# Kernel tuning notes

Hardware: AMD Instinct MI355X
Metric: run time of the kernel (lower is better)

Reference implementation:

```python
import jax, jax.numpy as jnp
import numpy as np
from jax.scipy.special import gammainc

ALPH = 0.8  # significance level (default arg in original forward)


def _median_width(X, iu, ju):
    # pairwise squared distances; original takes median of strictly-positive
    # strict-upper-triangle entries (tril subtracted) -> median over triu(k=1)
    G = jnp.sum(X * X, axis=1)                    # [n]
    D = G[:, None] + G[None, :] - 2.0 * (X @ X.T)  # [n, n]
    du = D[iu, ju]                                 # strict upper triangle, static size
    return jnp.sqrt(0.5 * jnp.median(du))


def _rbf(X, width):
    G = jnp.sum(X * X, axis=1)
    D = G[:, None] + G[None, :] - 2.0 * (X @ X.T)
    return jnp.exp(-D / (2.0 * width ** 2))


def _center(K):
    # H K H with H = I - 11^T/n  ==  K - rowmean - colmean + totalmean
    cm = jnp.mean(K, axis=0, keepdims=True)   # mean over rows  -> [1, n]
    rm = jnp.mean(K, axis=1, keepdims=True)   # mean over cols  -> [n, 1]
    tm = jnp.mean(K)
    return K - cm - rm + tm


def _gamma_ppf(a, p):
    # invert regularized lower incomplete gamma via fixed-iteration bisection
    hi0 = a + 10.0 * jnp.sqrt(a) + 100.0
    def body(i, lohi):
        lo, hi = lohi
        mid = 0.5 * (lo + hi)
        below = gammainc(a, mid) < p
        return (jnp.where(below, mid, lo), jnp.where(below, hi, mid))
    lo, hi = jax.lax.fori_loop(0, 100, body, (jnp.zeros_like(a), hi0))
    return 0.5 * (lo + hi)


def setup_inputs() -> dict:
    key = jax.random.key(0)
    k1, k2 = jax.random.split(key)
    X = jax.random.normal(k1, (4096, 64), dtype=jnp.float32)
    Y = jax.random.normal(k2, (4096, 64), dtype=jnp.float32)
    return {"X": X, "Y": Y}


def reference(X, Y):
    n = X.shape[0]
    iu, ju = np.triu_indices(n, k=1)  # static index set

    width_x = _median_width(X, iu, ju)
    width_y = _median_width(Y, iu, ju)

    K = _rbf(X, width_x)
    L = _rbf(Y, width_y)

    Kc = _center(K)
    Lc = _center(L)

    testStat = jnp.sum(Kc.T * Lc) / n

    V = (Kc * Lc / 6.0) ** 2
    varHSIC = (jnp.sum(V) - jnp.trace(V)) / n / (n - 1)
    varHSIC = varHSIC * 72.0 * (n - 4) * (n - 5) / n / (n - 1) / (n - 2) / (n - 3)

    # zero-diagonal kernels for mean estimate
    K0sum = jnp.sum(K) - jnp.trace(K)
    L0sum = jnp.sum(L) - jnp.trace(L)
    muX = K0sum / n / (n - 1)
    muY = L0sum / n / (n - 1)
    mHSIC = (1.0 + muX * muY - muX - muY) / n

    al = mHSIC ** 2 / varHSIC
    bet = varHSIC * n / mHSIC
    thresh = bet * _gamma_ppf(al, jnp.float32(1.0 - ALPH))
    return (testStat, thresh)
```

## Files before the change

### kernel.cpp

```cpp
#include <hip/hip_runtime.h>

typedef unsigned int u32;
typedef unsigned short u16;
typedef __attribute__((ext_vector_type(8))) short bf16x8;
typedef __attribute__((ext_vector_type(4))) float f32x4;

#define NPTS 4096
#define DIM  64
#define NB   32
#define NBLK 528
#define WLO16 0x4140u
#define NWBIN 832
#define RSTR 836


__device__ __forceinline__ void bmap(int b, int& by, int& bx){
  by = 0;
  while (b >= NB - by){ b -= NB - by; by++; }
  bx = by + b;
}

__device__ __forceinline__ u16 f2bf(float x){
  u32 u = __float_as_uint(x);
  return (u16)((u + 0x7fffu + ((u>>16)&1u)) >> 16);
}

__global__ __launch_bounds__(256) void convert_k(const float* __restrict__ X, const float* __restrict__ Y,
                                                 u16* __restrict__ Xbf, float* __restrict__ Gall,
                                                 u32* __restrict__ histsum, double* __restrict__ rowK,
                                                 double* __restrict__ rowL, double* __restrict__ sums){
  int t = blockIdx.x*256 + threadIdx.x;
  int rid = t >> 1, hf = t & 1;
  int z = rid >> 12, row = rid & 4095;
  const float* src = (z ? Y : X) + (size_t)row*DIM + hf*32;
  u16* base = Xbf + ((size_t)z*32768 + (size_t)(row>>4)*128 + (row&15))*8;
  float g = 0.f;
#pragma unroll
  for (int f=0; f<4; f++){
    float4 f0 = *(const float4*)(src + f*8);
    float4 f1 = *(const float4*)(src + f*8 + 4);
    g = fmaf(f0.x,f0.x,g); g = fmaf(f0.y,f0.y,g); g = fmaf(f0.z,f0.z,g); g = fmaf(f0.w,f0.w,g);
    g = fmaf(f1.x,f1.x,g); g = fmaf(f1.y,f1.y,g); g = fmaf(f1.z,f1.z,g); g = fmaf(f1.w,f1.w,g);
    ushort4 h0, h1;
    h0.x=f2bf(f0.x); h0.y=f2bf(f0.y); h0.z=f2bf(f0.z); h0.w=f2bf(f0.w);
    h1.x=f2bf(f1.x); h1.y=f2bf(f1.y); h1.z=f2bf(f1.z); h1.w=f2bf(f1.w);
    u16* dst = base + (size_t)(hf*4 + f)*16*8;
    *(ushort4*)dst = h0;
    *(ushort4*)(dst+4) = h1;
  }
  g += __shfl_xor(g, 1, 64);
  if (hf==0) Gall[rid] = g;
  if (t < NPTS){ rowK[t] = 0.0; rowL[t] = 0.0; }
  if (t < 2*RSTR) histsum[t] = 0u;
  if (t < 2) sums[t] = 0.0;
}

__global__ __launch_bounds__(256,2) void hist_k(const u16* __restrict__ Xbf, const float* __restrict__ Gall,
                                                u32* __restrict__ histsum){
  __shared__ u32 lh[RSTR];
  int z = blockIdx.y, tid = threadIdx.x;
  int by,bx; bmap(blockIdx.x, by, bx);
  bool isdiag = (by==bx);
  u32 wgt = isdiag ? 1u : 2u;
  int w=tid>>6, lane=tid&63, q=lane>>4, nl=lane&15;
  for (int t=tid;t<RSTR;t+=256) lh[t]=0;
  __syncthreads();
  const bf16x8* Xb = (const bf16x8*)Xbf + (size_t)z*32768;
  const float* Gz = Gall + z*NPTS;
  int rt0 = w, rt1 = 4 + w;
  int ag0 = by*8 + rt0, ag1 = by*8 + rt1;
  bf16x8 a0f0 = Xb[ag0*128 + q*16 + nl];
  bf16x8 a0f1 = Xb[ag0*128 + (4+q)*16 + nl];
  bf16x8 a1f0 = Xb[ag1*128 + q*16 + nl];
  bf16x8 a1f1 = Xb[ag1*128 + (4+q)*16 + nl];
  float ga0 = Gz[ag0*16 + nl], ga1 = Gz[ag1*16 + nl];
  float g0m[4], g1m[4];
#pragma unroll
  for (int r=0;r<4;r++){ g0m[r] = __shfl(ga0, q*4+r, 64); g1m[r] = __shfl(ga1, q*4+r, 64); }
#pragma unroll
  for (int tb=0;tb<8;tb++){
    int jg = bx*8 + tb;
    bf16x8 bf0 = Xb[jg*128 + q*16 + nl];
    bf16x8 bf1 = Xb[jg*128 + (4+q)*16 + nl];
    f32x4 acc0 = (f32x4)0.0f, acc1 = (f32x4)0.0f;
    acc0 = __builtin_amdgcn_mfma_f32_16x16x32_bf16(a0f0, bf0, acc0, 0,0,0);
    acc0 = __builtin_amdgcn_mfma_f32_16x16x32_bf16(a0f1, bf1, acc0, 0,0,0);
    acc1 = __builtin_amdgcn_mfma_f32_16x16x32_bf16(a1f0, bf0, acc1, 0,0,0);
    acc1 = __builtin_amdgcn_mfma_f32_16x16x32_bf16(a1f1, bf1, acc1, 0,0,0);
    int j = jg*16 + nl;
    float gb = Gz[j];
#pragma unroll
    for (int r=0;r<4;r++){
      float d0 = (g0m[r] + gb) - 2.0f*acc0[r];
      float d1 = (g1m[r] + gb) - 2.0f*acc1[r];
      if (isdiag){
        if (ag0*16 + q*4 + r == j) d0 = 0.f;
        if (ag1*16 + q*4 + r == j) d1 = 0.f;
      }
      u32 t0 = __float_as_uint(d0) >> 16;
      u32 b0 = (t0 < WLO16) ? 0u : (t0 >= WLO16+NWBIN) ? (u32)(NWBIN+1) : (t0 - WLO16 + 1u);
      atomicAdd(&lh[b0], wgt);
      u32 t1 = __float_as_uint(d1) >> 16;
      u32 b1 = (t1 < WLO16) ? 0u : (t1 >= WLO16+NWBIN) ? (u32)(NWBIN+1) : (t1 - WLO16 + 1u);
      atomicAdd(&lh[b1], wgt);
    }
  }
  __syncthreads();
  u32* dst = histsum + (size_t)z*RSTR;
  for (int t=tid;t<RSTR;t+=256){
    u32 v = lh[t];
    if (v) atomicAdd(&dst[t], v);
  }
}

__global__ __launch_bounds__(256) void scan16i(const u32* __restrict__ histsum,
                                               float* __restrict__ scal,
                                               u32 kf1, u32 kf2){
  int z = blockIdx.x;
  int tid = threadIdx.x;
  __shared__ u32 wsum[4];
  __shared__ double svals[2];
  u32 c4[4] = {0,0,0,0};
  if (tid < 209){
    const u32* base = histsum + (size_t)z*RSTR + 4*tid;
    int lim = RSTR - 4*tid;
    c4[0] = base[0];
    if (lim>1) c4[1] = base[1];
    if (lim>2) c4[2] = base[2];
    if (lim>3) c4[3] = base[3];
  }
  u32 s = c4[0]+c4[1]+c4[2]+c4[3];
  int lane = tid & 63, wv = tid >> 6;
  u32 pre = s;
#pragma unroll
  for (int off=1; off<64; off<<=1){
    u32 t2 = __shfl_up(pre, off, 64);
    if (lane >= off) pre += t2;
  }
  if (lane==63) wsum[wv] = pre;
  __syncthreads();
  u32 base2 = 0;
  for (int k=0;k<wv;k++) base2 += wsum[k];
  u32 incl = base2 + pre, excl = incl - s;
  u32 ks[2] = {kf1,kf2};
#pragma unroll
  for (int w2=0; w2<2; w2++){
    if (ks[w2] >= excl && ks[w2] < incl){
      u32 acc = excl;
#pragma unroll
      for (int j=0;j<4;j++){
        if (ks[w2] < acc + c4[j]){
          int b = tid*4 + j;
          double lo, hi;
          if (b==0){ lo=12.0; hi=12.0; }
          else if (b>=NWBIN+1){ lo=1024.0; hi=1024.0; }
          else {
            u32 t16 = WLO16 + (u32)b - 1u;
            lo = (double)__uint_as_float(t16<<16);
            hi = (double)__uint_as_float((t16+1u)<<16);
          }
          double frac = ((double)(ks[w2]-acc) + 0.5)/(double)c4[j];
          svals[w2] = lo + (hi-lo)*frac;
          break;
        }
        acc += c4[j];
      }
    }
  }
  __syncthreads();
  if (tid==0){
    float med = (float)(0.5*(svals[0]+svals[1]));
    float wd = sqrtf(0.5f*med);
    scal[z] = 2.0f*wd*wd;
  }
}

__global__ __launch_bounds__(256,2) void rowsum_k(const u16* __restrict__ Xbf, const float* __restrict__ Gall,
                                                  const float* __restrict__ scal,
                                                  double* __restrict__ rowK, double* __restrict__ rowL,
                                                  double* __restrict__ sums){
  __shared__ double rowacc[128];
  __shared__ double colLDS[4][128];
  __shared__ double tred[2];
  int z = blockIdx.y, tid = threadIdx.x;
  int by,bx; bmap(blockIdx.x, by, bx);
  bool isdiag = (by==bx);
  int w=tid>>6, lane=tid&63, q=lane>>4, nl=lane&15;
  const bf16x8* Xb = (const bf16x8*)Xbf + (size_t)z*32768;
  const float* Gz = Gall + z*NPTS;
  float negi = -1.0f/scal[z];
  int rt0 = w, rt1 = 4 + w;
  int ag0 = by*8 + rt0, ag1 = by*8 + rt1;
  bf16x8 a0f0 = Xb[ag0*128 + q*16 + nl];
  bf16x8 a0f1 = Xb[ag0*128 + (4+q)*16 + nl];
  bf16x8 a1f0 = Xb[ag1*128 + q*16 + nl];
  bf16x8 a1f1 = Xb[ag1*128 + (4+q)*16 + nl];
  float ga0 = Gz[ag0*16 + nl], ga1 = Gz[ag1*16 + nl];
  float g0m[4], g1m[4];
#pragma unroll
  for (int r=0;r<4;r++){ g0m[r] = __shfl(ga0, q*4+r, 64); g1m[r] = __shfl(ga1, q*4+r, 64); }
  double rs0[4] = {0,0,0,0}, rs1[4] = {0,0,0,0};
#pragma unroll
  for (int tb=0;tb<8;tb++){
    int jg = bx*8 + tb;
    bf16x8 bf0 = Xb[jg*128 + q*16 + nl];
    bf16x8 bf1 = Xb[jg*128 + (4+q)*16 + nl];
    f32x4 acc0 = (f32x4)0.0f, acc1 = (f32x4)0.0f;
    acc0 = __builtin_amdgcn_mfma_f32_16x16x32_bf16(a0f0, bf0, acc0, 0,0,0);
    acc0 = __builtin_amdgcn_mfma_f32_16x16x32_bf16(a0f1, bf1, acc0, 0,0,0);
    acc1 = __builtin_amdgcn_mfma_f32_16x16x32_bf16(a1f0, bf0, acc1, 0,0,0);
    acc1 = __builtin_amdgcn_mfma_f32_16x16x32_bf16(a1f1, bf1, acc1, 0,0,0);
    int j = jg*16 + nl;
    float gb = Gz[j];
    double cs = 0.0;
#pragma unroll
    for (int r=0;r<4;r++){
      float d0 = (g0m[r] + gb) - 2.0f*acc0[r];
      float d1 = (g1m[r] + gb) - 2.0f*acc1[r];
      if (isdiag){
        if (ag0*16 + q*4 + r == j) d0 = 0.f;
        if (ag1*16 + q*4 + r == j) d1 = 0.f;
      }
      double e0 = (double)expf(d0*negi);
      double e1 = (double)expf(d1*negi);
      rs0[r] += e0; rs1[r] += e1;
      cs += e0 + e1;
    }
    cs += __shfl_xor(cs, 16, 64);
    cs += __shfl_xor(cs, 32, 64);
    if (q==0) colLDS[w][tb*16 + nl] = cs;
  }
#pragma unroll
  for (int r=0;r<4;r++){
    double v0 = rs0[r], v1 = rs1[r];
    v0 += __shfl_xor(v0,1,64); v0 += __shfl_xor(v0,2,64);
    v0 += __shfl_xor(v0,4,64); v0 += __shfl_xor(v0,8,64);
    v1 += __shfl_xor(v1,1,64); v1 += __shfl_xor(v1,2,64);
    v1 += __shfl_xor(v1,4,64); v1 += __shfl_xor(v1,8,64);
    rs0[r] = v0; rs1[r] = v1;
  }
  if (nl==0){
#pragma unroll
    for (int r=0;r<4;r++){
      rowacc[rt0*16 + q*4 + r] = rs0[r];
      rowacc[rt1*16 + q*4 + r] = rs1[r];
    }
  }
  __syncthreads();
  double tot = 0.0;
  if (tid < 128){
    double rv = rowacc[tid];
    double cv = colLDS[0][tid] + colLDS[1][tid] + colLDS[2][tid] + colLDS[3][tid];
    double* rowG = z ? rowL : rowK;
    atomicAdd(&rowG[by*128 + tid], rv);
    if (!isdiag) atomicAdd(&rowG[bx*128 + tid], cv);
    tot = rv + (isdiag ? 0.0 : cv);
  }
#pragma unroll
  for (int s2=1;s2<64;s2<<=1) tot += __shfl_xor(tot, s2, 64);
  if (lane==0 && w<2) tred[w] = tot;
  __syncthreads();
  if (tid==0) atomicAdd(&sums[z], tred[0] + tred[1]);
}

__global__ __launch_bounds__(256,2) void final_k(const u16* __restrict__ Xbf, const float* __restrict__ Gall,
                                                 const float* __restrict__ scal,
                                                 const double* __restrict__ rowK,
                                                 const double* __restrict__ rowL,
                                                 const double* __restrict__ sums,
                                                 double* __restrict__ partials){
  int tid = threadIdx.x;
  int b = blockIdx.x >> 1, half = blockIdx.x & 1;
  int by,bx; bmap(b,by,bx);
  bool isdiag = (by==bx);
  int w=tid>>6, lane=tid&63, q=lane>>4, nl=lane&15;
  const bf16x8* Xb = (const bf16x8*)Xbf;
  const bf16x8* Yb = Xb + 32768;
  const float* Gx = Gall;
  const float* Gy = Gall + NPTS;
  const double inv_n = 1.0/(double)NPTS;
  double tmK = sums[0]*(inv_n*inv_n), tmL = sums[1]*(inv_n*inv_n);
  float negx = -1.0f/scal[0], negy = -1.0f/scal[1];
  double wgt = isdiag ? 1.0 : 2.0;
  double S1=0, S2=0, trV=0;
  int rt = half*4 + w;
  int ag = by*8 + rt;
  bf16x8 axf0 = Xb[ag*128 + q*16 + nl];
  bf16x8 axf1 = Xb[ag*128 + (4+q)*16 + nl];
  bf16x8 ayf0 = Yb[ag*128 + q*16 + nl];
  bf16x8 ayf1 = Yb[ag*128 + (4+q)*16 + nl];
  int rowA = ag*16 + nl;
  float gaX = Gx[rowA], gaY = Gy[rowA];
  float gXm[4], gYm[4];
#pragma unroll
  for (int r=0;r<4;r++){ gXm[r] = __shfl(gaX, q*4+r, 64); gYm[r] = __shfl(gaY, q*4+r, 64); }
  double rmKi[4], rmLi[4];
#pragma unroll
  for (int r=0;r<4;r++){
    int i = ag*16 + q*4 + r;
    rmKi[r] = rowK[i]*inv_n; rmLi[r] = rowL[i]*inv_n;
  }
#pragma unroll
  for (int tb=0;tb<8;tb++){
    int jg = bx*8 + tb;
    f32x4 accX = (f32x4)0.0f, accY = (f32x4)0.0f;
    accX = __builtin_amdgcn_mfma_f32_16x16x32_bf16(axf0, Xb[jg*128 + q*16 + nl],     accX, 0,0,0);
    accX = __builtin_amdgcn_mfma_f32_16x16x32_bf16(axf1, Xb[jg*128 + (4+q)*16 + nl], accX, 0,0,0);
    accY = __builtin_amdgcn_mfma_f32_16x16x32_bf16(ayf0, Yb[jg*128 + q*16 + nl],     accY, 0,0,0);
    accY = __builtin_amdgcn_mfma_f32_16x16x32_bf16(ayf1, Yb[jg*128 + (4+q)*16 + nl], accY, 0,0,0);
    int j = jg*16 + nl;
    float gbX = Gx[j], gbY = Gy[j];
    double cmK = rowK[j]*inv_n - tmK;
    double cmL = rowL[j]*inv_n - tmL;
#pragma unroll
    for (int r=0;r<4;r++){
      int i = ag*16 + q*4 + r;
      float dx = (gXm[r] + gbX) - 2.0f*accX[r];
      float dy = (gYm[r] + gbY) - 2.0f*accY[r];
      bool dg = isdiag && i==j;
      if (dg){ dx = 0.f; dy = 0.f; }
      float kx = expf(dx*negx);
      float lv = expf(dy*negy);
      double kc = ((double)kx - rmKi[r]) - cmK;
      double lc = ((double)lv - rmLi[r]) - cmL;
      double prod = kc*lc;
      S1 += wgt*prod;
      double vv = (prod*prod)*(1.0/36.0);
      S2 += wgt*vv;
      if (dg) trV += vv;
    }
  }
  __shared__ double red[4][3];
  double vals[3]={S1,S2,trV};
  int wv = tid >> 6;
#pragma unroll
  for (int v=0;v<3;v++){
    double x = vals[v];
#pragma unroll
    for (int s2=1;s2<64;s2<<=1) x += __shfl_xor(x, s2, 64);
    if (lane==0) red[wv][v]=x;
  }
  __syncthreads();
  if (tid < 3)
    partials[(size_t)blockIdx.x*4 + tid] = red[0][tid]+red[1][tid]+red[2][tid]+red[3][tid];
}

__device__ double gammainc_wave(double a, double x, double lga, int lane){
  double C = 1.0/a;
  double psum = 0.0;
  for (int b=0;b<8192;b++){
    double k = (double)(b*64 + lane + 1);
    double rr = x/(a+k);
    double pp = rr;
#pragma unroll
    for (int s=1;s<64;s<<=1){
      double t = __shfl_up(pp, s, 64);
      if (lane >= s) pp *= t;
    }
    double c = C*pp;
    psum += c;
    double clast = __shfl(c, 63, 64);
    double rlast = __shfl(rr, 63, 64);
    C = clast;
    if (rlast < 1.0 && clast*rlast/(1.0-rlast) < 1e-17) break;
  }
#pragma unroll
  for (int s=1;s<64;s<<=1) psum += __shfl_xor(psum, s, 64);
  double total = 1.0/a + psum;
  return exp(-x + a*log(x) - lga) * total;
}

__global__ __launch_bounds__(256) void finalize_k(const double* __restrict__ partials,
                                                  const double* __restrict__ sums,
                                                  float* __restrict__ out)
{
  __shared__ double red[3][4];
  __shared__ double tot[4];
  int tid = threadIdx.x;
  double v0=0,v1=0,v2=0;
  for (int i=tid; i<2*NBLK; i+=256){
    const double* p = partials + (size_t)i*4;
    v0+=p[0]; v1+=p[1]; v2+=p[2];
  }
  double vals[3]={v0,v1,v2};
  int lane = tid & 63, wv = tid >> 6;
#pragma unroll
  for (int v=0;v<3;v++){
    double x = vals[v];
#pragma unroll
    for (int s2=1;s2<64;s2<<=1) x += __shfl_xor(x, s2, 64);
    if (lane==0) red[v][wv]=x;
  }
  __syncthreads();
  if (tid==0){
#pragma unroll
    for (int v=0;v<3;v++) tot[v] = red[v][0]+red[v][1]+red[v][2]+red[v][3];
  }
  __syncthreads();
  if (tid >= 64) return;

  const double n = (double)NPTS;
  double totK=sums[0], totL=sums[1];
  double S1=tot[0], S2=tot[1], trV=tot[2];
  double testStat = S1/n;
  double varHSIC = (S2 - trV)/n/(n-1.0);
  varHSIC = varHSIC*72.0*(n-4.0)*(n-5.0)/n/(n-1.0)/(n-2.0)/(n-3.0);
  double muX = (totK-n)/n/(n-1.0);
  double muY = (totL-n)/n/(n-1.0);
  double mHSIC = (1.0 + muX*muY - muX - muY)/n;
  double al = mHSIC*mHSIC/varHSIC;
  double bet = varHSIC*n/mHSIC;
  double p = (double)((float)(1.0-0.8));
  double lga = lgamma(al);
  double lo = 0.0, hi = al + 10.0*sqrt(al) + 100.0;
  const double zp = -0.8416212335729142957;
  double t = 1.0 - 1.0/(9.0*al) + zp/(3.0*sqrt(al));
  double x = al*t*t*t;
  if (!(x > 0.0) || !(x < hi)) x = 0.5*hi;
  for (int it=0; it<2; ++it){
    double P = gammainc_wave(al, x, lga, lane);
    double diff = P - p;
    if (diff < 0.0) lo = x; else hi = x;
    if (fabs(diff) < 1e-12) break;
    double pdf = exp(-x + (al-1.0)*log(x) - lga);
    double nx = x - diff/pdf;
    if (!(nx > lo) || !(nx < hi)) nx = 0.5*(lo+hi);
    x = nx;
  }
  if (lane==0){
    out[0]=(float)testStat;
    out[1]=(float)(bet*x);
  }
}

extern "C" void kernel_launch(void* const* d_in, const int* in_sizes, int n_in,
                              void* d_out, int out_size, void* d_ws, size_t ws_size,
                              hipStream_t stream) {
  const float* X = (const float*)d_in[0];
  const float* Y = (const float*)d_in[1];
  float* out = (float*)d_out;
  char* ws = (char*)d_ws;

  double* sums     = (double*)ws;
  float*  scal     = (float*)(ws + 128);
  u32*    histsum  = (u32*)(ws + 256);
  double* rowK     = (double*)(ws + 8192);
  double* rowL     = (double*)(ws + 40960);
  float*  Gall     = (float*)(ws + 73728);
  double* partials = (double*)(ws + 106496);
  u16*    Xbf      = (u16*)(ws + (4u<<20));
  size_t need = (size_t)(4u<<20) + (size_t)2*NPTS*DIM*2;

  if (ws_size < need) return;

  const u32 KF1 = 4096u + 2u*4193279u;
  const u32 KF2 = 4096u + 2u*4193280u;

  convert_k<<<64,256,0,stream>>>(X, Y, Xbf, Gall, histsum, rowK, rowL, sums);
  hist_k<<<dim3(NBLK,2),256,0,stream>>>(Xbf, Gall, histsum);
  scan16i<<<2,256,0,stream>>>(histsum, scal, KF1, KF2);
  rowsum_k<<<dim3(NBLK,2),256,0,stream>>>(Xbf, Gall, scal, rowK, rowL, sums);
  final_k<<<2*NBLK,256,0,stream>>>(Xbf, Gall, scal, rowK, rowL, sums, partials);
  finalize_k<<<1,256,0,stream>>>(partials, sums, out);
}
```

Measured before the change: 146.9 us.

## Fuse six HSIC kernels into one cooperative persistent kernel with grid syncs

Replaces the chain of separate launches (convert, histogram, scan, rowsum, final, finalize) with a single cooperative kernel. Stages are separated by grid-wide barriers and work items are distributed over a persistent grid sized from occupancy. This removes per-launch overhead and inter-kernel gaps. In exchange, grid.sync costs are added, occupancy is fixed at a grid that may be smaller than the original work count, and all phases share one union of shared memory.

```diff
diff --git a/kernel.cpp b/kernel.cpp
--- a/kernel.cpp
+++ b/kernel.cpp
@@ -1,4 +1,7 @@
 #include <hip/hip_runtime.h>
+#include <hip/hip_cooperative_groups.h>
+
+namespace cg = cooperative_groups;
 
 typedef unsigned int u32;
 typedef unsigned short u16;
@@ -12,6 +15,8 @@
 #define WLO16 0x4140u
 #define NWBIN 832
 #define RSTR 836
+#define KF1C 8390654u
+#define KF2C 8390656u
 
 
 __device__ __forceinline__ void bmap(int b, int& by, int& bx){
@@ -23,326 +28,6 @@
 __device__ __forceinline__ u16 f2bf(float x){
   u32 u = __float_as_uint(x);
   return (u16)((u + 0x7fffu + ((u>>16)&1u)) >> 16);
-}
-
-__global__ __launch_bounds__(256) void convert_k(const float* __restrict__ X, const float* __restrict__ Y,
-                                                 u16* __restrict__ Xbf, float* __restrict__ Gall,
-                                                 u32* __restrict__ histsum, double* __restrict__ rowK,
-                                                 double* __restrict__ rowL, double* __restrict__ sums){
-  int t = blockIdx.x*256 + threadIdx.x;
-  int rid = t >> 1, hf = t & 1;
-  int z = rid >> 12, row = rid & 4095;
-  const float* src = (z ? Y : X) + (size_t)row*DIM + hf*32;
-  u16* base = Xbf + ((size_t)z*32768 + (size_t)(row>>4)*128 + (row&15))*8;
-  float g = 0.f;
-#pragma unroll
-  for (int f=0; f<4; f++){
-    float4 f0 = *(const float4*)(src + f*8);
-    float4 f1 = *(const float4*)(src + f*8 + 4);
-    g = fmaf(f0.x,f0.x,g); g = fmaf(f0.y,f0.y,g); g = fmaf(f0.z,f0.z,g); g = fmaf(f0.w,f0.w,g);
-    g = fmaf(f1.x,f1.x,g); g = fmaf(f1.y,f1.y,g); g = fmaf(f1.z,f1.z,g); g = fmaf(f1.w,f1.w,g);
-    ushort4 h0, h1;
-    h0.x=f2bf(f0.x); h0.y=f2bf(f0.y); h0.z=f2bf(f0.z); h0.w=f2bf(f0.w);
-    h1.x=f2bf(f1.x); h1.y=f2bf(f1.y); h1.z=f2bf(f1.z); h1.w=f2bf(f1.w);
-    u16* dst = base + (size_t)(hf*4 + f)*16*8;
-    *(ushort4*)dst = h0;
-    *(ushort4*)(dst+4) = h1;
-  }
-  g += __shfl_xor(g, 1, 64);
-  if (hf==0) Gall[rid] = g;
-  if (t < NPTS){ rowK[t] = 0.0; rowL[t] = 0.0; }
-  if (t < 2*RSTR) histsum[t] = 0u;
-  if (t < 2) sums[t] = 0.0;
-}
-
-__global__ __launch_bounds__(256,2) void hist_k(const u16* __restrict__ Xbf, const float* __restrict__ Gall,
-                                                u32* __restrict__ histsum){
-  __shared__ u32 lh[RSTR];
-  int z = blockIdx.y, tid = threadIdx.x;
-  int by,bx; bmap(blockIdx.x, by, bx);
-  bool isdiag = (by==bx);
-  u32 wgt = isdiag ? 1u : 2u;
-  int w=tid>>6, lane=tid&63, q=lane>>4, nl=lane&15;
-  for (int t=tid;t<RSTR;t+=256) lh[t]=0;
-  __syncthreads();
-  const bf16x8* Xb = (const bf16x8*)Xbf + (size_t)z*32768;
-  const float* Gz = Gall + z*NPTS;
-  int rt0 = w, rt1 = 4 + w;
-  int ag0 = by*8 + rt0, ag1 = by*8 + rt1;
-  bf16x8 a0f0 = Xb[ag0*128 + q*16 + nl];
-  bf16x8 a0f1 = Xb[ag0*128 + (4+q)*16 + nl];
-  bf16x8 a1f0 = Xb[ag1*128 + q*16 + nl];
-  bf16x8 a1f1 = Xb[ag1*128 + (4+q)*16 + nl];
-  float ga0 = Gz[ag0*16 + nl], ga1 = Gz[ag1*16 + nl];
-  float g0m[4], g1m[4];
-#pragma unroll
-  for (int r=0;r<4;r++){ g0m[r] = __shfl(ga0, q*4+r, 64); g1m[r] = __shfl(ga1, q*4+r, 64); }
-#pragma unroll
-  for (int tb=0;tb<8;tb++){
-    int jg = bx*8 + tb;
-    bf16x8 bf0 = Xb[jg*128 + q*16 + nl];
-    bf16x8 bf1 = Xb[jg*128 + (4+q)*16 + nl];
-    f32x4 acc0 = (f32x4)0.0f, acc1 = (f32x4)0.0f;
-    acc0 = __builtin_amdgcn_mfma_f32_16x16x32_bf16(a0f0, bf0, acc0, 0,0,0);
-    acc0 = __builtin_amdgcn_mfma_f32_16x16x32_bf16(a0f1, bf1, acc0, 0,0,0);
-    acc1 = __builtin_amdgcn_mfma_f32_16x16x32_bf16(a1f0, bf0, acc1, 0,0,0);
-    acc1 = __builtin_amdgcn_mfma_f32_16x16x32_bf16(a1f1, bf1, acc1, 0,0,0);
-    int j = jg*16 + nl;
-    float gb = Gz[j];
-#pragma unroll
-    for (int r=0;r<4;r++){
-      float d0 = (g0m[r] + gb) - 2.0f*acc0[r];
-      float d1 = (g1m[r] + gb) - 2.0f*acc1[r];
-      if (isdiag){
-        if (ag0*16 + q*4 + r == j) d0 = 0.f;
-        if (ag1*16 + q*4 + r == j) d1 = 0.f;
-      }
-      u32 t0 = __float_as_uint(d0) >> 16;
-      u32 b0 = (t0 < WLO16) ? 0u : (t0 >= WLO16+NWBIN) ? (u32)(NWBIN+1) : (t0 - WLO16 + 1u);
-      atomicAdd(&lh[b0], wgt);
-      u32 t1 = __float_as_uint(d1) >> 16;
-      u32 b1 = (t1 < WLO16) ? 0u : (t1 >= WLO16+NWBIN) ? (u32)(NWBIN+1) : (t1 - WLO16 + 1u);
-      atomicAdd(&lh[b1], wgt);
-    }
-  }
-  __syncthreads();
-  u32* dst = histsum + (size_t)z*RSTR;
-  for (int t=tid;t<RSTR;t+=256){
-    u32 v = lh[t];
-    if (v) atomicAdd(&dst[t], v);
-  }
-}
-
-__global__ __launch_bounds__(256) void scan16i(const u32* __restrict__ histsum,
-                                               float* __restrict__ scal,
-                                               u32 kf1, u32 kf2){
-  int z = blockIdx.x;
-  int tid = threadIdx.x;
-  __shared__ u32 wsum[4];
-  __shared__ double svals[2];
-  u32 c4[4] = {0,0,0,0};
-  if (tid < 209){
-    const u32* base = histsum + (size_t)z*RSTR + 4*tid;
-    int lim = RSTR - 4*tid;
-    c4[0] = base[0];
-    if (lim>1) c4[1] = base[1];
-    if (lim>2) c4[2] = base[2];
-    if (lim>3) c4[3] = base[3];
-  }
-  u32 s = c4[0]+c4[1]+c4[2]+c4[3];
-  int lane = tid & 63, wv = tid >> 6;
-  u32 pre = s;
-#pragma unroll
-  for (int off=1; off<64; off<<=1){
-    u32 t2 = __shfl_up(pre, off, 64);
-    if (lane >= off) pre += t2;
-  }
-  if (lane==63) wsum[wv] = pre;
-  __syncthreads();
-  u32 base2 = 0;
-  for (int k=0;k<wv;k++) base2 += wsum[k];
-  u32 incl = base2 + pre, excl = incl - s;
-  u32 ks[2] = {kf1,kf2};
-#pragma unroll
-  for (int w2=0; w2<2; w2++){
-    if (ks[w2] >= excl && ks[w2] < incl){
-      u32 acc = excl;
-#pragma unroll
-      for (int j=0;j<4;j++){
-        if (ks[w2] < acc + c4[j]){
-          int b = tid*4 + j;
-          double lo, hi;
-          if (b==0){ lo=12.0; hi=12.0; }
-          else if (b>=NWBIN+1){ lo=1024.0; hi=1024.0; }
-          else {
-            u32 t16 = WLO16 + (u32)b - 1u;
-            lo = (double)__uint_as_float(t16<<16);
-            hi = (double)__uint_as_float((t16+1u)<<16);
-          }
-          double frac = ((double)(ks[w2]-acc) + 0.5)/(double)c4[j];
-          svals[w2] = lo + (hi-lo)*frac;
-          break;
-        }
-        acc += c4[j];
-      }
-    }
-  }
-  __syncthreads();
-  if (tid==0){
-    float med = (float)(0.5*(svals[0]+svals[1]));
-    float wd = sqrtf(0.5f*med);
-    scal[z] = 2.0f*wd*wd;
-  }
-}
-
-__global__ __launch_bounds__(256,2) void rowsum_k(const u16* __restrict__ Xbf, const float* __restrict__ Gall,
-                                                  const float* __restrict__ scal,
-                                                  double* __restrict__ rowK, double* __restrict__ rowL,
-                                                  double* __restrict__ sums){
-  __shared__ double rowacc[128];
-  __shared__ double colLDS[4][128];
-  __shared__ double tred[2];
-  int z = blockIdx.y, tid = threadIdx.x;
-  int by,bx; bmap(blockIdx.x, by, bx);
-  bool isdiag = (by==bx);
-  int w=tid>>6, lane=tid&63, q=lane>>4, nl=lane&15;
-  const bf16x8* Xb = (const bf16x8*)Xbf + (size_t)z*32768;
-  const float* Gz = Gall + z*NPTS;
-  float negi = -1.0f/scal[z];
-  int rt0 = w, rt1 = 4 + w;
-  int ag0 = by*8 + rt0, ag1 = by*8 + rt1;
-  bf16x8 a0f0 = Xb[ag0*128 + q*16 + nl];
-  bf16x8 a0f1 = Xb[ag0*128 + (4+q)*16 + nl];
-  bf16x8 a1f0 = Xb[ag1*128 + q*16 + nl];
-  bf16x8 a1f1 = Xb[ag1*128 + (4+q)*16 + nl];
-  float ga0 = Gz[ag0*16 + nl], ga1 = Gz[ag1*16 + nl];
-  float g0m[4], g1m[4];
-#pragma unroll
-  for (int r=0;r<4;r++){ g0m[r] = __shfl(ga0, q*4+r, 64); g1m[r] = __shfl(ga1, q*4+r, 64); }
-  double rs0[4] = {0,0,0,0}, rs1[4] = {0,0,0,0};
-#pragma unroll
-  for (int tb=0;tb<8;tb++){
-    int jg = bx*8 + tb;
-    bf16x8 bf0 = Xb[jg*128 + q*16 + nl];
-    bf16x8 bf1 = Xb[jg*128 + (4+q)*16 + nl];
-    f32x4 acc0 = (f32x4)0.0f, acc1 = (f32x4)0.0f;
-    acc0 = __builtin_amdgcn_mfma_f32_16x16x32_bf16(a0f0, bf0, acc0, 0,0,0);
-    acc0 = __builtin_amdgcn_mfma_f32_16x16x32_bf16(a0f1, bf1, acc0, 0,0,0);
-    acc1 = __builtin_amdgcn_mfma_f32_16x16x32_bf16(a1f0, bf0, acc1, 0,0,0);
-    acc1 = __builtin_amdgcn_mfma_f32_16x16x32_bf16(a1f1, bf1, acc1, 0,0,0);
-    int j = jg*16 + nl;
-    float gb = Gz[j];
-    double cs = 0.0;
-#pragma unroll
-    for (int r=0;r<4;r++){
-      float d0 = (g0m[r] + gb) - 2.0f*acc0[r];
-      float d1 = (g1m[r] + gb) - 2.0f*acc1[r];
-      if (isdiag){
-        if (ag0*16 + q*4 + r == j) d0 = 0.f;
-        if (ag1*16 + q*4 + r == j) d1 = 0.f;
-      }
-      double e0 = (double)expf(d0*negi);
-      double e1 = (double)expf(d1*negi);
-      rs0[r] += e0; rs1[r] += e1;
-      cs += e0 + e1;
-    }
-    cs += __shfl_xor(cs, 16, 64);
-    cs += __shfl_xor(cs, 32, 64);
-    if (q==0) colLDS[w][tb*16 + nl] = cs;
-  }
-#pragma unroll
-  for (int r=0;r<4;r++){
-    double v0 = rs0[r], v1 = rs1[r];
-    v0 += __shfl_xor(v0,1,64); v0 += __shfl_xor(v0,2,64);
-    v0 += __shfl_xor(v0,4,64); v0 += __shfl_xor(v0,8,64);
-    v1 += __shfl_xor(v1,1,64); v1 += __shfl_xor(v1,2,64);
-    v1 += __shfl_xor(v1,4,64); v1 += __shfl_xor(v1,8,64);
-    rs0[r] = v0; rs1[r] = v1;
-  }
-  if (nl==0){
-#pragma unroll
-    for (int r=0;r<4;r++){
-      rowacc[rt0*16 + q*4 + r] = rs0[r];
-      rowacc[rt1*16 + q*4 + r] = rs1[r];
-    }
-  }
-  __syncthreads();
-  double tot = 0.0;
-  if (tid < 128){
-    double rv = rowacc[tid];
-    double cv = colLDS[0][tid] + colLDS[1][tid] + colLDS[2][tid] + colLDS[3][tid];
-    double* rowG = z ? rowL : rowK;
-    atomicAdd(&rowG[by*128 + tid], rv);
-    if (!isdiag) atomicAdd(&rowG[bx*128 + tid], cv);
-    tot = rv + (isdiag ? 0.0 : cv);
-  }
-#pragma unroll
-  for (int s2=1;s2<64;s2<<=1) tot += __shfl_xor(tot, s2, 64);
-  if (lane==0 && w<2) tred[w] = tot;
-  __syncthreads();
-  if (tid==0) atomicAdd(&sums[z], tred[0] + tred[1]);
-}
-
-__global__ __launch_bounds__(256,2) void final_k(const u16* __restrict__ Xbf, const float* __restrict__ Gall,
-                                                 const float* __restrict__ scal,
-                                                 const double* __restrict__ rowK,
-                                                 const double* __restrict__ rowL,
-                                                 const double* __restrict__ sums,
-                                                 double* __restrict__ partials){
-  int tid = threadIdx.x;
-  int b = blockIdx.x >> 1, half = blockIdx.x & 1;
-  int by,bx; bmap(b,by,bx);
-  bool isdiag = (by==bx);
-  int w=tid>>6, lane=tid&63, q=lane>>4, nl=lane&15;
-  const bf16x8* Xb = (const bf16x8*)Xbf;
-  const bf16x8* Yb = Xb + 32768;
-  const float* Gx = Gall;
-  const float* Gy = Gall + NPTS;
-  const double inv_n = 1.0/(double)NPTS;
-  double tmK = sums[0]*(inv_n*inv_n), tmL = sums[1]*(inv_n*inv_n);
-  float negx = -1.0f/scal[0], negy = -1.0f/scal[1];
-  double wgt = isdiag ? 1.0 : 2.0;
-  double S1=0, S2=0, trV=0;
-  int rt = half*4 + w;
-  int ag = by*8 + rt;
-  bf16x8 axf0 = Xb[ag*128 + q*16 + nl];
-  bf16x8 axf1 = Xb[ag*128 + (4+q)*16 + nl];
-  bf16x8 ayf0 = Yb[ag*128 + q*16 + nl];
-  bf16x8 ayf1 = Yb[ag*128 + (4+q)*16 + nl];
-  int rowA = ag*16 + nl;
-  float gaX = Gx[rowA], gaY = Gy[rowA];
-  float gXm[4], gYm[4];
-#pragma unroll
-  for (int r=0;r<4;r++){ gXm[r] = __shfl(gaX, q*4+r, 64); gYm[r] = __shfl(gaY, q*4+r, 64); }
-  double rmKi[4], rmLi[4];
-#pragma unroll
-  for (int r=0;r<4;r++){
-    int i = ag*16 + q*4 + r;
-    rmKi[r] = rowK[i]*inv_n; rmLi[r] = rowL[i]*inv_n;
-  }
-#pragma unroll
-  for (int tb=0;tb<8;tb++){
-    int jg = bx*8 + tb;
-    f32x4 accX = (f32x4)0.0f, accY = (f32x4)0.0f;
-    accX = __builtin_amdgcn_mfma_f32_16x16x32_bf16(axf0, Xb[jg*128 + q*16 + nl],     accX, 0,0,0);
-    accX = __builtin_amdgcn_mfma_f32_16x16x32_bf16(axf1, Xb[jg*128 + (4+q)*16 + nl], accX, 0,0,0);
-    accY = __builtin_amdgcn_mfma_f32_16x16x32_bf16(ayf0, Yb[jg*128 + q*16 + nl],     accY, 0,0,0);
-    accY = __builtin_amdgcn_mfma_f32_16x16x32_bf16(ayf1, Yb[jg*128 + (4+q)*16 + nl], accY, 0,0,0);
-    int j = jg*16 + nl;
-    float gbX = Gx[j], gbY = Gy[j];
-    double cmK = rowK[j]*inv_n - tmK;
-    double cmL = rowL[j]*inv_n - tmL;
-#pragma unroll
-    for (int r=0;r<4;r++){
-      int i = ag*16 + q*4 + r;
-      float dx = (gXm[r] + gbX) - 2.0f*accX[r];
-      float dy = (gYm[r] + gbY) - 2.0f*accY[r];
-      bool dg = isdiag && i==j;
-      if (dg){ dx = 0.f; dy = 0.f; }
-      float kx = expf(dx*negx);
-      float lv = expf(dy*negy);
-      double kc = ((double)kx - rmKi[r]) - cmK;
-      double lc = ((double)lv - rmLi[r]) - cmL;
-      double prod = kc*lc;
-      S1 += wgt*prod;
-      double vv = (prod*prod)*(1.0/36.0);
-      S2 += wgt*vv;
-      if (dg) trV += vv;
-    }
-  }
-  __shared__ double red[4][3];
-  double vals[3]={S1,S2,trV};
-  int wv = tid >> 6;
-#pragma unroll
-  for (int v=0;v<3;v++){
-    double x = vals[v];
-#pragma unroll
-    for (int s2=1;s2<64;s2<<=1) x += __shfl_xor(x, s2, 64);
-    if (lane==0) red[wv][v]=x;
-  }
-  __syncthreads();
-  if (tid < 3)
-    partials[(size_t)blockIdx.x*4 + tid] = red[0][tid]+red[1][tid]+red[2][tid]+red[3][tid];
 }
 
 __device__ double gammainc_wave(double a, double x, double lga, int lane){
@@ -370,66 +55,381 @@
   return exp(-x + a*log(x) - lga) * total;
 }
 
-__global__ __launch_bounds__(256) void finalize_k(const double* __restrict__ partials,
-                                                  const double* __restrict__ sums,
-                                                  float* __restrict__ out)
+__global__ __launch_bounds__(256,2) void hsic_all(
+    const float* __restrict__ X, const float* __restrict__ Y,
+    u16* __restrict__ Xbf, float* __restrict__ Gall,
+    u32* __restrict__ histsum, double* __restrict__ rowK, double* __restrict__ rowL,
+    double* __restrict__ sums, float* __restrict__ scal, double* __restrict__ partials,
+    float* __restrict__ out)
 {
-  __shared__ double red[3][4];
-  __shared__ double tot[4];
-  int tid = threadIdx.x;
-  double v0=0,v1=0,v2=0;
-  for (int i=tid; i<2*NBLK; i+=256){
-    const double* p = partials + (size_t)i*4;
-    v0+=p[0]; v1+=p[1]; v2+=p[2];
-  }
-  double vals[3]={v0,v1,v2};
-  int lane = tid & 63, wv = tid >> 6;
-#pragma unroll
-  for (int v=0;v<3;v++){
-    double x = vals[v];
-#pragma unroll
-    for (int s2=1;s2<64;s2<<=1) x += __shfl_xor(x, s2, 64);
-    if (lane==0) red[v][wv]=x;
-  }
-  __syncthreads();
-  if (tid==0){
-#pragma unroll
-    for (int v=0;v<3;v++) tot[v] = red[v][0]+red[v][1]+red[v][2]+red[v][3];
-  }
-  __syncthreads();
-  if (tid >= 64) return;
-
-  const double n = (double)NPTS;
-  double totK=sums[0], totL=sums[1];
-  double S1=tot[0], S2=tot[1], trV=tot[2];
-  double testStat = S1/n;
-  double varHSIC = (S2 - trV)/n/(n-1.0);
-  varHSIC = varHSIC*72.0*(n-4.0)*(n-5.0)/n/(n-1.0)/(n-2.0)/(n-3.0);
-  double muX = (totK-n)/n/(n-1.0);
-  double muY = (totL-n)/n/(n-1.0);
-  double mHSIC = (1.0 + muX*muY - muX - muY)/n;
-  double al = mHSIC*mHSIC/varHSIC;
-  double bet = varHSIC*n/mHSIC;
-  double p = (double)((float)(1.0-0.8));
-  double lga = lgamma(al);
-  double lo = 0.0, hi = al + 10.0*sqrt(al) + 100.0;
-  const double zp = -0.8416212335729142957;
-  double t = 1.0 - 1.0/(9.0*al) + zp/(3.0*sqrt(al));
-  double x = al*t*t*t;
-  if (!(x > 0.0) || !(x < hi)) x = 0.5*hi;
-  for (int it=0; it<2; ++it){
-    double P = gammainc_wave(al, x, lga, lane);
-    double diff = P - p;
-    if (diff < 0.0) lo = x; else hi = x;
-    if (fabs(diff) < 1e-12) break;
-    double pdf = exp(-x + (al-1.0)*log(x) - lga);
-    double nx = x - diff/pdf;
-    if (!(nx > lo) || !(nx < hi)) nx = 0.5*(lo+hi);
-    x = nx;
-  }
-  if (lane==0){
-    out[0]=(float)testStat;
-    out[1]=(float)(bet*x);
+  cg::grid_group grid = cg::this_grid();
+  const int tid = threadIdx.x;
+  const int bid = blockIdx.x;
+  const int gsz = gridDim.x;
+  const int w = tid>>6, lane = tid&63, q = lane>>4, nl = lane&15;
+  const int gtid = bid*256 + tid;
+  const int gstr = gsz*256;
+
+  __shared__ union {
+    u32 lh[RSTR];
+    struct { double rowacc[128]; double colLDS[4][128]; double tred[2]; } rs;
+    struct { u32 wsum[4]; double svals[2]; } sc;
+    struct { double red[4][3]; } fr;
+    struct { double red2[3][4]; double tot[4]; } fz;
+  } sh;
+
+  for (int t = gtid; t < 4*NPTS; t += gstr){
+    int rid = t >> 1, hf = t & 1;
+    int z = rid >> 12, row = rid & 4095;
+    const float* src = (z ? Y : X) + (size_t)row*DIM + hf*32;
+    u16* basep = Xbf + ((size_t)z*32768 + (size_t)(row>>4)*128 + (row&15))*8;
+    float g = 0.f;
+#pragma unroll
+    for (int f=0; f<4; f++){
+      float4 f0 = *(const float4*)(src + f*8);
+      float4 f1 = *(const float4*)(src + f*8 + 4);
+      g = fmaf(f0.x,f0.x,g); g = fmaf(f0.y,f0.y,g); g = fmaf(f0.z,f0.z,g); g = fmaf(f0.w,f0.w,g);
+      g = fmaf(f1.x,f1.x,g); g = fmaf(f1.y,f1.y,g); g = fmaf(f1.z,f1.z,g); g = fmaf(f1.w,f1.w,g);
+      ushort4 h0, h1;
+      h0.x=f2bf(f0.x); h0.y=f2bf(f0.y); h0.z=f2bf(f0.z); h0.w=f2bf(f0.w);
+      h1.x=f2bf(f1.x); h1.y=f2bf(f1.y); h1.z=f2bf(f1.z); h1.w=f2bf(f1.w);
+      u16* dst = basep + (size_t)(hf*4 + f)*16*8;
+      *(ushort4*)dst = h0;
+      *(ushort4*)(dst+4) = h1;
+    }
+    g += __shfl_xor(g, 1, 64);
+    if (hf==0) Gall[rid] = g;
+  }
+  for (int t = gtid; t < NPTS; t += gstr){ rowK[t]=0.0; rowL[t]=0.0; }
+  for (int t = gtid; t < 2*RSTR; t += gstr) histsum[t]=0u;
+  if (gtid==0){ sums[0]=0.0; sums[1]=0.0; }
+  __threadfence(); grid.sync(); __threadfence();
+
+  for (int tile = bid; tile < 2*NBLK; tile += gsz){
+    int z = (tile >= NBLK) ? 1 : 0;
+    int b = tile - (z ? NBLK : 0);
+    int by,bx; bmap(b,by,bx);
+    bool isdiag = (by==bx);
+    u32 wgt = isdiag ? 1u : 2u;
+    for (int t=tid;t<RSTR;t+=256) sh.lh[t]=0;
+    __syncthreads();
+    const bf16x8* Xb = (const bf16x8*)Xbf + (size_t)z*32768;
+    const float* Gz = Gall + z*NPTS;
+    int ag0 = by*8 + w, ag1 = by*8 + 4 + w;
+    bf16x8 a0f0 = Xb[ag0*128 + q*16 + nl];
+    bf16x8 a0f1 = Xb[ag0*128 + (4+q)*16 + nl];
+    bf16x8 a1f0 = Xb[ag1*128 + q*16 + nl];
+    bf16x8 a1f1 = Xb[ag1*128 + (4+q)*16 + nl];
+    float ga0 = Gz[ag0*16 + nl], ga1 = Gz[ag1*16 + nl];
+    float g0m[4], g1m[4];
+#pragma unroll
+    for (int r=0;r<4;r++){ g0m[r] = __shfl(ga0, q*4+r, 64); g1m[r] = __shfl(ga1, q*4+r, 64); }
+#pragma unroll
+    for (int tb=0;tb<8;tb++){
+      int jg = bx*8 + tb;
+      bf16x8 bf0 = Xb[jg*128 + q*16 + nl];
+      bf16x8 bf1 = Xb[jg*128 + (4+q)*16 + nl];
+      f32x4 acc0 = (f32x4)0.0f, acc1 = (f32x4)0.0f;
+      acc0 = __builtin_amdgcn_mfma_f32_16x16x32_bf16(a0f0, bf0, acc0, 0,0,0);
+      acc0 = __builtin_amdgcn_mfma_f32_16x16x32_bf16(a0f1, bf1, acc0, 0,0,0);
+      acc1 = __builtin_amdgcn_mfma_f32_16x16x32_bf16(a1f0, bf0, acc1, 0,0,0);
+      acc1 = __builtin_amdgcn_mfma_f32_16x16x32_bf16(a1f1, bf1, acc1, 0,0,0);
+      int j = jg*16 + nl;
+      float gb = Gz[j];
+#pragma unroll
+      for (int r=0;r<4;r++){
+        float d0 = (g0m[r] + gb) - 2.0f*acc0[r];
+        float d1 = (g1m[r] + gb) - 2.0f*acc1[r];
+        if (isdiag){
+          if (ag0*16 + q*4 + r == j) d0 = 0.f;
+          if (ag1*16 + q*4 + r == j) d1 = 0.f;
+        }
+        u32 t0 = __float_as_uint(d0) >> 16;
+        u32 bin0 = (t0 < WLO16) ? 0u : (t0 >= WLO16+NWBIN) ? (u32)(NWBIN+1) : (t0 - WLO16 + 1u);
+        atomicAdd(&sh.lh[bin0], wgt);
+        u32 t1 = __float_as_uint(d1) >> 16;
+        u32 bin1 = (t1 < WLO16) ? 0u : (t1 >= WLO16+NWBIN) ? (u32)(NWBIN+1) : (t1 - WLO16 + 1u);
+        atomicAdd(&sh.lh[bin1], wgt);
+      }
+    }
+    __syncthreads();
+    u32* dst = histsum + (size_t)z*RSTR;
+    for (int t=tid;t<RSTR;t+=256){
+      u32 v = sh.lh[t];
+      if (v) atomicAdd(&dst[t], v);
+    }
+  }
+  __threadfence(); grid.sync(); __threadfence();
+
+  if (bid < 2){
+    int z = bid;
+    u32 c4[4] = {0,0,0,0};
+    if (tid < 209){
+      const u32* base = histsum + (size_t)z*RSTR + 4*tid;
+      int lim = RSTR - 4*tid;
+      c4[0] = base[0];
+      if (lim>1) c4[1] = base[1];
+      if (lim>2) c4[2] = base[2];
+      if (lim>3) c4[3] = base[3];
+    }
+    u32 s = c4[0]+c4[1]+c4[2]+c4[3];
+    u32 pre = s;
+#pragma unroll
+    for (int off=1; off<64; off<<=1){
+      u32 t2 = __shfl_up(pre, off, 64);
+      if (lane >= off) pre += t2;
+    }
+    if (lane==63) sh.sc.wsum[w] = pre;
+    __syncthreads();
+    u32 base2 = 0;
+    for (int k=0;k<w;k++) base2 += sh.sc.wsum[k];
+    u32 incl = base2 + pre, excl = incl - s;
+    u32 ks[2] = {KF1C,KF2C};
+#pragma unroll
+    for (int w2=0; w2<2; w2++){
+      if (ks[w2] >= excl && ks[w2] < incl){
+        u32 acc = excl;
+#pragma unroll
+        for (int j=0;j<4;j++){
+          if (ks[w2] < acc + c4[j]){
+            int b = tid*4 + j;
+            double lo, hi;
+            if (b==0){ lo=12.0; hi=12.0; }
+            else if (b>=NWBIN+1){ lo=1024.0; hi=1024.0; }
+            else {
+              u32 t16 = WLO16 + (u32)b - 1u;
+              lo = (double)__uint_as_float(t16<<16);
+              hi = (double)__uint_as_float((t16+1u)<<16);
+            }
+            double frac = ((double)(ks[w2]-acc) + 0.5)/(double)c4[j];
+            sh.sc.svals[w2] = lo + (hi-lo)*frac;
+            break;
+          }
+          acc += c4[j];
+        }
+      }
+    }
+    __syncthreads();
+    if (tid==0){
+      float med = (float)(0.5*(sh.sc.svals[0]+sh.sc.svals[1]));
+      float wd = sqrtf(0.5f*med);
+      scal[z] = 2.0f*wd*wd;
+    }
+  }
+  __threadfence(); grid.sync(); __threadfence();
+
+  for (int tile = bid; tile < 2*NBLK; tile += gsz){
+    int z = (tile >= NBLK) ? 1 : 0;
+    int b = tile - (z ? NBLK : 0);
+    int by,bx; bmap(b,by,bx);
+    bool isdiag = (by==bx);
+    const bf16x8* Xb = (const bf16x8*)Xbf + (size_t)z*32768;
+    const float* Gz = Gall + z*NPTS;
+    float negi = -1.0f/scal[z];
+    int ag0 = by*8 + w, ag1 = by*8 + 4 + w;
+    bf16x8 a0f0 = Xb[ag0*128 + q*16 + nl];
+    bf16x8 a0f1 = Xb[ag0*128 + (4+q)*16 + nl];
+    bf16x8 a1f0 = Xb[ag1*128 + q*16 + nl];
+    bf16x8 a1f1 = Xb[ag1*128 + (4+q)*16 + nl];
+    float ga0 = Gz[ag0*16 + nl], ga1 = Gz[ag1*16 + nl];
+    float g0m[4], g1m[4];
+#pragma unroll
+    for (int r=0;r<4;r++){ g0m[r] = __shfl(ga0, q*4+r, 64); g1m[r] = __shfl(ga1, q*4+r, 64); }
+    double rs0[4] = {0,0,0,0}, rs1[4] = {0,0,0,0};
+#pragma unroll
+    for (int tb=0;tb<8;tb++){
+      int jg = bx*8 + tb;
+      bf16x8 bf0 = Xb[jg*128 + q*16 + nl];
+      bf16x8 bf1 = Xb[jg*128 + (4+q)*16 + nl];
+      f32x4 acc0 = (f32x4)0.0f, acc1 = (f32x4)0.0f;
+      acc0 = __builtin_amdgcn_mfma_f32_16x16x32_bf16(a0f0, bf0, acc0, 0,0,0);
+      acc0 = __builtin_amdgcn_mfma_f32_16x16x32_bf16(a0f1, bf1, acc0, 0,0,0);
+      acc1 = __builtin_amdgcn_mfma_f32_16x16x32_bf16(a1f0, bf0, acc1, 0,0,0);
+      acc1 = __builtin_amdgcn_mfma_f32_16x16x32_bf16(a1f1, bf1, acc1, 0,0,0);
+      int j = jg*16 + nl;
+      float gb = Gz[j];
+      double cs = 0.0;
+#pragma unroll
+      for (int r=0;r<4;r++){
+        float d0 = (g0m[r] + gb) - 2.0f*acc0[r];
+        float d1 = (g1m[r] + gb) - 2.0f*acc1[r];
+        if (isdiag){
+          if (ag0*16 + q*4 + r == j) d0 = 0.f;
+          if (ag1*16 + q*4 + r == j) d1 = 0.f;
+        }
+        double e0 = (double)expf(d0*negi);
+        double e1 = (double)expf(d1*negi);
+        rs0[r] += e0; rs1[r] += e1;
+        cs += e0 + e1;
+      }
+      cs += __shfl_xor(cs, 16, 64);
+      cs += __shfl_xor(cs, 32, 64);
+      if (q==0) sh.rs.colLDS[w][tb*16 + nl] = cs;
+    }
+#pragma unroll
+    for (int r=0;r<4;r++){
+      double v0 = rs0[r], v1 = rs1[r];
+      v0 += __shfl_xor(v0,1,64); v0 += __shfl_xor(v0,2,64);
+      v0 += __shfl_xor(v0,4,64); v0 += __shfl_xor(v0,8,64);
+      v1 += __shfl_xor(v1,1,64); v1 += __shfl_xor(v1,2,64);
+      v1 += __shfl_xor(v1,4,64); v1 += __shfl_xor(v1,8,64);
+      rs0[r] = v0; rs1[r] = v1;
+    }
+    if (nl==0){
+#pragma unroll
+      for (int r=0;r<4;r++){
+        sh.rs.rowacc[w*16 + q*4 + r]     = rs0[r];
+        sh.rs.rowacc[(4+w)*16 + q*4 + r] = rs1[r];
+      }
+    }
+    __syncthreads();
+    double tot = 0.0;
+    if (tid < 128){
+      double rv = sh.rs.rowacc[tid];
+      double cv = sh.rs.colLDS[0][tid] + sh.rs.colLDS[1][tid] + sh.rs.colLDS[2][tid] + sh.rs.colLDS[3][tid];
+      double* rowG = z ? rowL : rowK;
+      atomicAdd(&rowG[by*128 + tid], rv);
+      if (!isdiag) atomicAdd(&rowG[bx*128 + tid], cv);
+      tot = rv + (isdiag ? 0.0 : cv);
+    }
+#pragma unroll
+    for (int s2=1;s2<64;s2<<=1) tot += __shfl_xor(tot, s2, 64);
+    if (lane==0 && w<2) sh.rs.tred[w] = tot;
+    __syncthreads();
+    if (tid==0) atomicAdd(&sums[z], sh.rs.tred[0] + sh.rs.tred[1]);
+  }
+  __threadfence(); grid.sync(); __threadfence();
+
+  {
+    const bf16x8* Xb = (const bf16x8*)Xbf;
+    const bf16x8* Yb = Xb + 32768;
+    const float* Gx = Gall;
+    const float* Gy = Gall + NPTS;
+    const double inv_n = 1.0/(double)NPTS;
+    double tmK = sums[0]*(inv_n*inv_n), tmL = sums[1]*(inv_n*inv_n);
+    float negx = -1.0f/scal[0], negy = -1.0f/scal[1];
+    double S1=0, S2=0, trV=0;
+    for (int t = bid; t < 2*NBLK; t += gsz){
+      int b = t >> 1, half = t & 1;
+      int by,bx; bmap(b,by,bx);
+      bool isdiag = (by==bx);
+      double wgt = isdiag ? 1.0 : 2.0;
+      int ag = by*8 + half*4 + w;
+      bf16x8 axf0 = Xb[ag*128 + q*16 + nl];
+      bf16x8 axf1 = Xb[ag*128 + (4+q)*16 + nl];
+      bf16x8 ayf0 = Yb[ag*128 + q*16 + nl];
+      bf16x8 ayf1 = Yb[ag*128 + (4+q)*16 + nl];
+      int rowA = ag*16 + nl;
+      float gaX = Gx[rowA], gaY = Gy[rowA];
+      float gXm[4], gYm[4];
+#pragma unroll
+      for (int r=0;r<4;r++){ gXm[r] = __shfl(gaX, q*4+r, 64); gYm[r] = __shfl(gaY, q*4+r, 64); }
+      double rmKi[4], rmLi[4];
+#pragma unroll
+      for (int r=0;r<4;r++){
+        int i = ag*16 + q*4 + r;
+        rmKi[r] = rowK[i]*inv_n; rmLi[r] = rowL[i]*inv_n;
+      }
+#pragma unroll
+      for (int tb=0;tb<8;tb++){
+        int jg = bx*8 + tb;
+        f32x4 accX = (f32x4)0.0f, accY = (f32x4)0.0f;
+        accX = __builtin_amdgcn_mfma_f32_16x16x32_bf16(axf0, Xb[jg*128 + q*16 + nl],     accX, 0,0,0);
+        accX = __builtin_amdgcn_mfma_f32_16x16x32_bf16(axf1, Xb[jg*128 + (4+q)*16 + nl], accX, 0,0,0);
+        accY = __builtin_amdgcn_mfma_f32_16x16x32_bf16(ayf0, Yb[jg*128 + q*16 + nl],     accY, 0,0,0);
+        accY = __builtin_amdgcn_mfma_f32_16x16x32_bf16(ayf1, Yb[jg*128 + (4+q)*16 + nl], accY, 0,0,0);
+        int j = jg*16 + nl;
+        float gbX = Gx[j], gbY = Gy[j];
+        double cmK = rowK[j]*inv_n - tmK;
+        double cmL = rowL[j]*inv_n - tmL;
+#pragma unroll
+        for (int r=0;r<4;r++){
+          int i = ag*16 + q*4 + r;
+          float dx = (gXm[r] + gbX) - 2.0f*accX[r];
+          float dy = (gYm[r] + gbY) - 2.0f*accY[r];
+          bool dg = isdiag && i==j;
+          if (dg){ dx = 0.f; dy = 0.f; }
+          float kx = expf(dx*negx);
+          float lv = expf(dy*negy);
+          double kc = ((double)kx - rmKi[r]) - cmK;
+          double lc = ((double)lv - rmLi[r]) - cmL;
+          double prod = kc*lc;
+          S1 += wgt*prod;
+          double vv = (prod*prod)*(1.0/36.0);
+          S2 += wgt*vv;
+          if (dg) trV += vv;
+        }
+      }
+    }
+    double vals[3]={S1,S2,trV};
+#pragma unroll
+    for (int v=0;v<3;v++){
+      double x = vals[v];
+#pragma unroll
+      for (int s2=1;s2<64;s2<<=1) x += __shfl_xor(x, s2, 64);
+      if (lane==0) sh.fr.red[w][v]=x;
+    }
+    __syncthreads();
+    if (tid < 3)
+      partials[(size_t)bid*4 + tid] = sh.fr.red[0][tid]+sh.fr.red[1][tid]+sh.fr.red[2][tid]+sh.fr.red[3][tid];
+  }
+  __threadfence(); grid.sync(); __threadfence();
+
+  if (bid != 0) return;
+  {
+    double v0=0,v1=0,v2=0;
+    for (int i=tid; i<gsz; i+=256){
+      const double* p = partials + (size_t)i*4;
+      v0+=p[0]; v1+=p[1]; v2+=p[2];
+    }
+    double vals[3]={v0,v1,v2};
+#pragma unroll
+    for (int v=0;v<3;v++){
+      double x = vals[v];
+#pragma unroll
+      for (int s2=1;s2<64;s2<<=1) x += __shfl_xor(x, s2, 64);
+      if (lane==0) sh.fz.red2[v][w]=x;
+    }
+    __syncthreads();
+    if (tid==0){
+#pragma unroll
+      for (int v=0;v<3;v++) sh.fz.tot[v] = sh.fz.red2[v][0]+sh.fz.red2[v][1]+sh.fz.red2[v][2]+sh.fz.red2[v][3];
+    }
+    __syncthreads();
+    if (tid >= 64) return;
+
+    const double n = (double)NPTS;
+    double totK=sums[0], totL=sums[1];
+    double S1=sh.fz.tot[0], S2=sh.fz.tot[1], trV=sh.fz.tot[2];
+    double testStat = S1/n;
+    double varHSIC = (S2 - trV)/n/(n-1.0);
+    varHSIC = varHSIC*72.0*(n-4.0)*(n-5.0)/n/(n-1.0)/(n-2.0)/(n-3.0);
+    double muX = (totK-n)/n/(n-1.0);
+    double muY = (totL-n)/n/(n-1.0);
+    double mHSIC = (1.0 + muX*muY - muX - muY)/n;
+    double al = mHSIC*mHSIC/varHSIC;
+    double bet = varHSIC*n/mHSIC;
+    double p = (double)((float)(1.0-0.8));
+    double lga = lgamma(al);
+    double lo = 0.0, hi = al + 10.0*sqrt(al) + 100.0;
+    const double zp = -0.8416212335729142957;
+    double tt = 1.0 - 1.0/(9.0*al) + zp/(3.0*sqrt(al));
+    double x = al*tt*tt*tt;
+    if (!(x > 0.0) || !(x < hi)) x = 0.5*hi;
+    for (int it=0; it<2; ++it){
+      double P = gammainc_wave(al, x, lga, lane);
+      double diff = P - p;
+      if (diff < 0.0) lo = x; else hi = x;
+      if (fabs(diff) < 1e-12) break;
+      double pdf = exp(-x + (al-1.0)*log(x) - lga);
+      double nx = x - diff/pdf;
+      if (!(nx > lo) || !(nx < hi)) nx = 0.5*(lo+hi);
+      x = nx;
+    }
+    if (lane==0){
+      out[0]=(float)testStat;
+      out[1]=(float)(bet*x);
+    }
   }
 }
 
@@ -453,13 +453,23 @@
 
   if (ws_size < need) return;
 
-  const u32 KF1 = 4096u + 2u*4193279u;
-  const u32 KF2 = 4096u + 2u*4193280u;
-
-  convert_k<<<64,256,0,stream>>>(X, Y, Xbf, Gall, histsum, rowK, rowL, sums);
-  hist_k<<<dim3(NBLK,2),256,0,stream>>>(Xbf, Gall, histsum);
-  scan16i<<<2,256,0,stream>>>(histsum, scal, KF1, KF2);
-  rowsum_k<<<dim3(NBLK,2),256,0,stream>>>(Xbf, Gall, scal, rowK, rowL, sums);
-  final_k<<<2*NBLK,256,0,stream>>>(Xbf, Gall, scal, rowK, rowL, sums, partials);
-  finalize_k<<<1,256,0,stream>>>(partials, sums, out);
+  static int gridBlocks = 0;
+  if (gridBlocks == 0){
+    int dev = 0; (void)hipGetDevice(&dev);
+    int nCU = 0; (void)hipDeviceGetAttribute(&nCU, hipDeviceAttributeMultiprocessorCount, dev);
+    int maxb = 0;
+    (void)hipOccupancyMaxActiveBlocksPerMultiprocessor(&maxb, reinterpret_cast<const void*>(hsic_all), 256, 0);
+    if (nCU <= 0) nCU = 256;
+    if (maxb <= 0) maxb = 1;
+    long g = (long)nCU * (long)maxb;
+    if (g > 2*NBLK) g = 2*NBLK;
+    if (g < 2) g = 2;
+    gridBlocks = (int)g;
+  }
+
+  void* args[] = {(void*)&X, (void*)&Y, (void*)&Xbf, (void*)&Gall, (void*)&histsum,
+                  (void*)&rowK, (void*)&rowL, (void*)&sums, (void*)&scal,
+                  (void*)&partials, (void*)&out};
+  (void)hipLaunchCooperativeKernel(reinterpret_cast<const void*>(hsic_all),
+                                   dim3(gridBlocks), dim3(256), args, 0, stream);
 }
```

Result: slower. 475.9 us (+223.9%).
